# Optimization experiments

Measured on AMD Instinct MI355X. Metric: run time of the kernel, lower is better.

The kernel has to match this reference:

```python
import jax, jax.numpy as jnp
import numpy as np

N_CODES = 1024
CODE_DIM = 64
COMMITMENT_WEIGHT = 0.5
DECAY = 0.99
EPSILON = 1e-05
TEMP = 1.0


def setup_inputs() -> dict:
    key = jax.random.key(0)
    k_z, k_e = jax.random.split(key)
    z = jax.random.normal(k_z, (8, 16384, CODE_DIM), dtype=jnp.float32)
    # xavier_uniform init for embedding [n_codes, code_dim]
    limit = float(np.sqrt(6.0 / (N_CODES + CODE_DIM)))
    embedding = jax.random.uniform(k_e, (N_CODES, CODE_DIM), dtype=jnp.float32,
                                   minval=-limit, maxval=limit)
    ema_cluster_size = jnp.zeros((N_CODES,), dtype=jnp.float32)
    ema_w = embedding.copy()
    return {"z": z, "embedding": embedding,
            "ema_cluster_size": ema_cluster_size, "ema_w": ema_w}


def reference(z, embedding, ema_cluster_size, ema_w):
    lead_shape = z.shape[:-1]
    zf = z.reshape(-1, z.shape[-1])  # [N, D]
    # squared-euclidean distances: ||z||^2 + ||e||^2 - 2 z e^T  -> [N, n_codes]
    d = (jnp.sum(zf * zf, axis=-1, keepdims=True)
         + jnp.sum(embedding * embedding, axis=-1)
         - 2.0 * (zf @ embedding.T)) / TEMP
    idx = jnp.argmin(d, axis=-1)  # [N]
    z_q_f = embedding[idx]        # [N, D]

    # --- EMA codebook update (no-grad buffer math) ---
    ones = jnp.ones_like(idx, dtype=zf.dtype)
    cluster_size = jax.ops.segment_sum(ones, idx, num_segments=N_CODES)      # one_hot.sum(0)
    new_ecs = ema_cluster_size * DECAY + (1.0 - DECAY) * cluster_size
    n = jnp.sum(new_ecs)
    cs = jnp.clip((new_ecs + EPSILON) / (n + N_CODES * EPSILON) * n, 0.01)
    dw = jax.ops.segment_sum(zf, idx, num_segments=N_CODES)                  # one_hot.T @ z
    new_ema_w = ema_w * DECAY + (1.0 - DECAY) * dw
    new_embedding = new_ema_w / cs[:, None]

    # --- losses (straight-through) ---
    z_q = z_q_f.reshape(z.shape)
    commitment_loss = jnp.mean((jax.lax.stop_gradient(z_q) - z) ** 2)
    codebook_loss = jnp.mean((z_q - jax.lax.stop_gradient(z)) ** 2)
    loss = commitment_loss * COMMITMENT_WEIGHT + codebook_loss
    z_q_st = z + jax.lax.stop_gradient(z_q - z)

    # --- perplexity (no-grad) ---
    avg_probs = cluster_size / jnp.sum(cluster_size)
    avg_probs = jnp.clip(avg_probs, 1e-10)
    avg_probs = avg_probs / jnp.sum(avg_probs)
    perplexity = jnp.exp(-jnp.sum(avg_probs * jnp.log(avg_probs)))

    encoding_indices = idx.reshape(lead_shape)
    return (z_q_st, encoding_indices, loss, perplexity,
            new_embedding, new_ecs, new_ema_w)
```

## Files before the change

### kernel.cpp

```cpp
#include <hip/hip_runtime.h>
#include <hip/hip_bf16.h>
#include <math.h>

#define N_ROWS   131072
#define DIMS     64
#define NCODES   1024
#define DECAY    0.99f
#define EPSF     1e-5f
#define BAND     2e-3f

#define OFF_ZQ    0
#define OFF_IDX   8388608
#define OFF_LOSS  8519680
#define OFF_PERP  8519681
#define OFF_EMB   8519682
#define OFF_ECS   8585218
#define OFF_EMAW  8586242

typedef unsigned int uint;
typedef short bf16x8 __attribute__((ext_vector_type(8)));
typedef float f32x4  __attribute__((ext_vector_type(4)));

__device__ __forceinline__ float atomic_add_f32(float* p, float v) {
  return __hip_atomic_fetch_add(p, v, __ATOMIC_RELAXED, __HIP_MEMORY_SCOPE_AGENT);
}

__device__ __forceinline__ unsigned short bf16_rne(float f) {
  uint u = __float_as_uint(f);
  uint r = u + 0x7fffu + ((u >> 16) & 1u);
  return (unsigned short)(r >> 16);
}
__device__ __forceinline__ float bf16_f32(unsigned short h) {
  return __uint_as_float(((uint)h) << 16);
}

__device__ __forceinline__ float np_pairwise64_sq(const float* v) {
#pragma clang fp contract(off)
  float r[8];
#pragma unroll
  for (int j = 0; j < 8; ++j) r[j] = v[j] * v[j];
#pragma unroll
  for (int i = 8; i < 64; i += 8)
#pragma unroll
    for (int j = 0; j < 8; ++j) r[j] += v[i + j] * v[i + j];
  return ((r[0] + r[1]) + (r[2] + r[3])) + ((r[4] + r[5]) + (r[6] + r[7]));
}

__global__ __launch_bounds__(256) void k0m(const float* __restrict__ emb,
                                           float* __restrict__ ee,
                                           uint* __restrict__ cluster,
                                           uint* __restrict__ cnt,
                                           bf16x8* __restrict__ bsplit,
                                           float* __restrict__ dw) {
  int T = blockIdx.x;
  int t = threadIdx.x;
  int gid = T * 256 + t;
  for (int i = gid; i < NCODES * DIMS; i += 16384) dw[i] = 0.0f;

  int l = t & 63;
  int slot = t >> 6;
  int ktile = slot >> 1, split = slot & 1;
  int code = T * 16 + (l & 15);
  int k0 = ktile * 32 + ((l >> 4) << 3);
  const float* ep = emb + (size_t)code * DIMS + k0;
  float4 fa = *(const float4*)ep;
  float4 fb = *(const float4*)(ep + 4);
  float fs[8] = {fa.x, fa.y, fa.z, fa.w, fb.x, fb.y, fb.z, fb.w};
  bf16x8 v;
#pragma unroll
  for (int i = 0; i < 8; ++i) {
    unsigned short h = bf16_rne(fs[i]);
    if (split == 0) v[i] = (short)h;
    else            v[i] = (short)bf16_rne(fs[i] - bf16_f32(h));
  }
  bsplit[(size_t)((T * 2 + ktile) * 2 + split) * 64 + l] = v;

  if (t < 16) {
    int c = T * 16 + t;
    float ev[DIMS];
    const float4* e4 = (const float4*)(emb + (size_t)c * DIMS);
#pragma unroll
    for (int i = 0; i < 16; ++i) {
      float4 w = e4[i];
      ev[4*i] = w.x; ev[4*i+1] = w.y; ev[4*i+2] = w.z; ev[4*i+3] = w.w;
    }
    ee[c] = np_pairwise64_sq(ev);
  } else if (t < 32) {
    cluster[T * 16 + (t - 16)] = 0u;
  }
  if (T == 0 && t == 32) *cnt = 0u;
}

__global__ __launch_bounds__(256) void k1_mfma(const float* __restrict__ z,
                                               const float* __restrict__ emb,
                                               const bf16x8* __restrict__ bsplit,
                                               const float* __restrict__ ee,
                                               int* __restrict__ idx_out,
                                               float* __restrict__ idx_f_out,
                                               float* __restrict__ out_zq,
                                               double* __restrict__ sqpart,
                                               uint* __restrict__ cluster,
                                               uint* __restrict__ cnt,
                                               uint* __restrict__ list) {
  __shared__ float4 btile[4][256];
  __shared__ int    sidx[64];
  __shared__ double wred[4];
  int t = threadIdx.x;
  int l = t & 63;
  int w = t >> 6;
  int rowbase = blockIdx.x * 64 + w * 16;
  int arow = rowbase + (l & 15);
  int kq = (l >> 4) << 3;
  int col = l & 15;

  const float4* bs4 = (const float4*)bsplit;

  bf16x8 ahi[2], ami[2];
#pragma unroll
  for (int t2 = 0; t2 < 2; ++t2) {
    const float* zp = z + (size_t)arow * DIMS + t2 * 32 + kq;
    float4 fa = *(const float4*)zp;
    float4 fb = *(const float4*)(zp + 4);
    float fs[8] = {fa.x, fa.y, fa.z, fa.w, fb.x, fb.y, fb.z, fb.w};
#pragma unroll
    for (int i = 0; i < 8; ++i) {
      unsigned short h = bf16_rne(fs[i]);
      float m = fs[i] - bf16_f32(h);
      ahi[t2][i] = (short)bf16_rne(-2.0f * fs[i]);
      ami[t2][i] = (short)bf16_rne(-2.0f * m);
    }
  }

  float best[4]  = {3.4e38f, 3.4e38f, 3.4e38f, 3.4e38f};
  float second[4] = {3.4e38f, 3.4e38f, 3.4e38f, 3.4e38f};
  int   bidx[4] = {0, 0, 0, 0};

  float4 vp0 = bs4[(size_t)(0 * 4 + w) * 64 + l];
  float4 vp1 = bs4[(size_t)(1 * 4 + w) * 64 + l];
  float4 vp2 = bs4[(size_t)(2 * 4 + w) * 64 + l];
  float4 vp3 = bs4[(size_t)(3 * 4 + w) * 64 + l];

  for (int T = 0; T < 64; T += 4) {
    __syncthreads();
    btile[0][w * 64 + l] = vp0;
    btile[1][w * 64 + l] = vp1;
    btile[2][w * 64 + l] = vp2;
    btile[3][w * 64 + l] = vp3;
    __syncthreads();
    if (T + 4 < 64) {
      vp0 = bs4[(size_t)((T + 4) * 4 + w) * 64 + l];
      vp1 = bs4[(size_t)((T + 5) * 4 + w) * 64 + l];
      vp2 = bs4[(size_t)((T + 6) * 4 + w) * 64 + l];
      vp3 = bs4[(size_t)((T + 7) * 4 + w) * 64 + l];
    }

#pragma unroll
    for (int u = 0; u < 4; ++u) {
      int code = (T + u) * 16 + col;
      float eeT = ee[code];
      bf16x8 bhi0 = __builtin_bit_cast(bf16x8, btile[u][0 * 64 + l]);
      bf16x8 bmi0 = __builtin_bit_cast(bf16x8, btile[u][1 * 64 + l]);
      bf16x8 bhi1 = __builtin_bit_cast(bf16x8, btile[u][2 * 64 + l]);
      bf16x8 bmi1 = __builtin_bit_cast(bf16x8, btile[u][3 * 64 + l]);

      f32x4 acc = {0.f, 0.f, 0.f, 0.f};
      acc = __builtin_amdgcn_mfma_f32_16x16x32_bf16(ahi[0], bhi0, acc, 0, 0, 0);
      acc = __builtin_amdgcn_mfma_f32_16x16x32_bf16(ahi[1], bhi1, acc, 0, 0, 0);
      acc = __builtin_amdgcn_mfma_f32_16x16x32_bf16(ahi[0], bmi0, acc, 0, 0, 0);
      acc = __builtin_amdgcn_mfma_f32_16x16x32_bf16(ahi[1], bmi1, acc, 0, 0, 0);
      acc = __builtin_amdgcn_mfma_f32_16x16x32_bf16(ami[0], bhi0, acc, 0, 0, 0);
      acc = __builtin_amdgcn_mfma_f32_16x16x32_bf16(ami[1], bhi1, acc, 0, 0, 0);

#pragma unroll
      for (int j = 0; j < 4; ++j) {
        float s = acc[j] + eeT;
        bool lt = s < best[j];
        second[j] = lt ? best[j] : fminf(second[j], s);
        best[j]   = lt ? s : best[j];
        bidx[j]   = lt ? code : bidx[j];
      }
    }
  }

#pragma unroll
  for (int m = 1; m < 16; m <<= 1) {
#pragma unroll
    for (int j = 0; j < 4; ++j) {
      float ob = __shfl_xor(best[j], m, 64);
      float os = __shfl_xor(second[j], m, 64);
      int   oi = __shfl_xor(bidx[j], m, 64);
      if (ob < best[j]) {
        second[j] = fminf(os, best[j]);
        best[j] = ob; bidx[j] = oi;
      } else if (ob == best[j]) {
        bidx[j] = min(bidx[j], oi);
        second[j] = fminf(second[j], fminf(os, ob));
      } else {
        second[j] = fminf(second[j], ob);
      }
    }
  }

  if (col == 0) {
#pragma unroll
    for (int j = 0; j < 4; ++j) {
      int lrow = w * 16 + ((l >> 4) << 2) + j;
      int r = blockIdx.x * 64 + lrow;
      sidx[lrow] = bidx[j];
      idx_out[r] = bidx[j];
      idx_f_out[r] = (float)bidx[j];
      atomicAdd(&cluster[bidx[j]], 1u);
      if (second[j] - best[j] < BAND) {
        uint p = atomicAdd(cnt, 1u);
        list[p] = (uint)r;
      }
    }
  }
  __syncthreads();

  double ds = 0.0;
  const float4* z4 = (const float4*)z;
  const float4* e4 = (const float4*)emb;
  float4* zq4 = (float4*)out_zq;
  int blockrow = blockIdx.x * 64;
#pragma unroll
  for (int p = 0; p < 4; ++p) {
    int f = t + p * 256;
    int lrow = f >> 4, d4 = f & 15;
    int code = sidx[lrow];
    float4 zv = z4[(size_t)(blockrow + lrow) * 16 + d4];
    float4 ev = e4[code * 16 + d4];
    float dx = ev.x - zv.x, dy = ev.y - zv.y, dz = ev.z - zv.z, dw_ = ev.w - zv.w;
    float4 o;
    o.x = zv.x + dx; o.y = zv.y + dy; o.z = zv.z + dz; o.w = zv.w + dw_;
    zq4[(size_t)(blockrow + lrow) * 16 + d4] = o;
    float ss = dx * dx + dy * dy + dz * dz + dw_ * dw_;
    ds += (double)ss;
  }
#pragma unroll
  for (int o2 = 32; o2 > 0; o2 >>= 1) ds += __shfl_down(ds, o2, 64);
  if (l == 0) wred[w] = ds;
  __syncthreads();
  if (t == 0) sqpart[blockIdx.x] = (wred[0] + wred[1]) + (wred[2] + wred[3]);
}

__global__ __launch_bounds__(256) void k2_recheck(const float* __restrict__ z,
                                                  const float* __restrict__ emb,
                                                  const float* __restrict__ ee,
                                                  const uint* __restrict__ cnt,
                                                  const uint* __restrict__ list,
                                                  int* __restrict__ idx_out,
                                                  float* __restrict__ idx_f_out,
                                                  float* __restrict__ out_zq,
                                                  uint* __restrict__ cluster,
                                                  double* __restrict__ corr) {
#pragma clang fp contract(off)
  __shared__ float zrow[DIMS];
  __shared__ float rv[256];
  __shared__ int   ri[256];
  __shared__ int   schg, sold, snew;
  int t = threadIdx.x;
  uint n = *cnt;
  double corrAcc = 0.0;
  const float4* e4 = (const float4*)emb;
  float4* zq4 = (float4*)out_zq;

  for (uint i = blockIdx.x; i < n; i += gridDim.x) {
    uint row = list[i];
    __syncthreads();
    if (t < 16)
      ((float4*)zrow)[t] = ((const float4*)(z + (size_t)row * DIMS))[t];
    __syncthreads();
    float zz = np_pairwise64_sq(zrow);
    float best = 3.4e38f; int bi = 0;
#pragma unroll
    for (int k4 = 0; k4 < 4; ++k4) {
      int c = t * 4 + k4;
      const float* e = emb + (size_t)c * DIMS;
      float a = 0.f;
      for (int k = 0; k < DIMS; ++k) a = fmaf(zrow[k], e[k], a);
      float d = fmaf(-2.0f, a, zz + ee[c]);
      if (d < best) { best = d; bi = c; }
    }
    rv[t] = best; ri[t] = bi;
    __syncthreads();
    for (int s = 128; s > 0; s >>= 1) {
      if (t < s) {
        float ov = rv[t + s]; int oi = ri[t + s];
        if (ov < rv[t] || (ov == rv[t] && oi < ri[t])) { rv[t] = ov; ri[t] = oi; }
      }
      __syncthreads();
    }
    if (t == 0) {
      int old = idx_out[row];
      if (ri[0] != old) {
        atomicSub(&cluster[old], 1u);
        atomicAdd(&cluster[ri[0]], 1u);
        idx_out[row] = ri[0];
        idx_f_out[row] = (float)ri[0];
        schg = 1; sold = old; snew = ri[0];
      } else {
        schg = 0;
      }
    }
    __syncthreads();
    if (schg && t < 16) {
      float4 zv = make_float4(zrow[t*4], zrow[t*4+1], zrow[t*4+2], zrow[t*4+3]);
      float4 en = e4[snew * 16 + t];
      float4 eo = e4[sold * 16 + t];
      float dxn = en.x - zv.x, dyn = en.y - zv.y, dzn = en.z - zv.z, dwn = en.w - zv.w;
      float4 o;
      o.x = zv.x + dxn; o.y = zv.y + dyn; o.z = zv.z + dzn; o.w = zv.w + dwn;
      zq4[(size_t)row * 16 + t] = o;
      float ssn = dxn * dxn + dyn * dyn + dzn * dzn + dwn * dwn;
      float dxo = eo.x - zv.x, dyo = eo.y - zv.y, dzo = eo.z - zv.z, dwo = eo.w - zv.w;
      float sso = dxo * dxo + dyo * dyo + dzo * dzo + dwo * dwo;
      double cl = (double)ssn - (double)sso;
      cl += __shfl_xor(cl, 1, 64);
      cl += __shfl_xor(cl, 2, 64);
      cl += __shfl_xor(cl, 4, 64);
      cl += __shfl_xor(cl, 8, 64);
      if (t == 0) corrAcc += cl;
    }
  }
  if (t == 0) corr[blockIdx.x] = corrAcc;
}

__global__ __launch_bounds__(256) void kp(const uint* __restrict__ cluster,
                                          const float* __restrict__ ecs_in,
                                          uint* __restrict__ starts,
                                          uint* __restrict__ cursor,
                                          float* __restrict__ csb,
                                          float* __restrict__ out) {
  __shared__ uint a[256], b[256];
  __shared__ double red[256];
  int t = threadIdx.x;

  uint c0 = cluster[t*4+0], c1 = cluster[t*4+1], c2 = cluster[t*4+2], c3 = cluster[t*4+3];
  uint s4 = c0 + c1 + c2 + c3;
  a[t] = s4;
  __syncthreads();
  uint* src = a; uint* dst = b;
  for (int off = 1; off < 256; off <<= 1) {
    dst[t] = src[t] + ((t >= off) ? src[t - off] : 0u);
    __syncthreads();
    uint* tmp = src; src = dst; dst = tmp;
  }
  uint base = (t > 0) ? src[t-1] : 0u;
  uint p0 = base, p1 = p0 + c0, p2 = p1 + c1, p3 = p2 + c2;
  starts[t*4+0] = p0; starts[t*4+1] = p1; starts[t*4+2] = p2; starts[t*4+3] = p3;
  cursor[t*4+0] = p0; cursor[t*4+1] = p1; cursor[t*4+2] = p2; cursor[t*4+3] = p3;
  if (t == 255) starts[NCODES] = src[255];
  __syncthreads();

  double nloc = 0.0, aloc = 0.0, bloc = 0.0;
  for (int c = t; c < NCODES; c += 256) {
    float cntf = (float)cluster[c];
    float ne = ecs_in[c] * DECAY + (1.0f - DECAY) * cntf;
    out[OFF_ECS + c] = ne;
    nloc += (double)ne;
    double p = (double)cntf / (double)N_ROWS;
    double pc = p < 1e-10 ? 1e-10 : p;
    bloc += pc;
    aloc += pc * log(pc);
  }

  red[t] = nloc; __syncthreads();
  for (int s = 128; s > 0; s >>= 1) { if (t < s) red[t] += red[t + s]; __syncthreads(); }
  double n = red[0]; __syncthreads();

  red[t] = bloc; __syncthreads();
  for (int s = 128; s > 0; s >>= 1) { if (t < s) red[t] += red[t + s]; __syncthreads(); }
  double B = red[0]; __syncthreads();

  red[t] = aloc; __syncthreads();
  for (int s = 128; s > 0; s >>= 1) { if (t < s) red[t] += red[t + s]; __syncthreads(); }
  double A = red[0]; __syncthreads();

  if (t == 0) {
    double ent = -(A / B - log(B));
    out[OFF_PERP] = (float)exp(ent);
  }

  float nf = (float)n;
  for (int c = t; c < NCODES; c += 256) {
    float ne = out[OFF_ECS + c];
    float cs = ((ne + EPSF) / (nf + (float)NCODES * EPSF)) * nf;
    csb[c] = cs < 0.01f ? 0.01f : cs;
  }
}

__global__ __launch_bounds__(256) void k3c_scatter(const int* __restrict__ idx,
                                                   uint* __restrict__ cursor,
                                                   uint* __restrict__ rowids,
                                                   int* __restrict__ codes) {
  int row = blockIdx.x * 256 + threadIdx.x;
  int code = idx[row];
  uint pos = atomicAdd(&cursor[code], 1u);
  rowids[pos] = (uint)row;
  codes[pos] = code;
}

__global__ __launch_bounds__(256) void k3d_dw(const float* __restrict__ z,
                                              const uint* __restrict__ rowids,
                                              const int* __restrict__ codes,
                                              float* __restrict__ dw) {
  int lane = threadIdx.x & 63, w = threadIdx.x >> 6;
  int base = blockIdx.x * 128 + w * 32;

  int cur = codes[base];
  float acc = 0.f;
  for (int i = 0; i < 32; ++i) {
    int p = base + i;
    uint r = rowids[p];
    int c = codes[p];
    if (c != cur) {
      atomic_add_f32(&dw[cur * DIMS + lane], acc);
      acc = 0.f; cur = c;
    }
    acc += z[(size_t)r * DIMS + lane];
  }
  atomic_add_f32(&dw[cur * DIMS + lane], acc);
}

__global__ __launch_bounds__(256) void k4b_emb(const float* __restrict__ emaw_in,
                                               const float* __restrict__ dw,
                                               const float* __restrict__ csb,
                                               const double* __restrict__ sqpart,
                                               const double* __restrict__ corr,
                                               float* __restrict__ out) {
  int i = blockIdx.x * 256 + threadIdx.x;
  int c = i >> 6;
  float nw = emaw_in[i] * DECAY + (1.0f - DECAY) * dw[i];
  out[OFF_EMAW + i] = nw;
  out[OFF_EMB + i] = nw / csb[c];

  if (blockIdx.x == 0) {
    __shared__ double red[256];
    int t = threadIdx.x;
    double sloc = 0.0;
    for (int k = t; k < 2048; k += 256) sloc += sqpart[k];
    for (int k = t; k < 1024; k += 256) sloc += corr[k];
    red[t] = sloc; __syncthreads();
    for (int s = 128; s > 0; s >>= 1) { if (t < s) red[t] += red[t + s]; __syncthreads(); }
    if (t == 0) {
      double M = red[0] / (double)((size_t)N_ROWS * DIMS);
      out[OFF_LOSS] = (float)(1.5 * M);
    }
  }
}

extern "C" void kernel_launch(void* const* d_in, const int* in_sizes, int n_in,
                              void* d_out, int out_size, void* d_ws, size_t ws_size,
                              hipStream_t stream) {
  const float* z    = (const float*)d_in[0];
  const float* emb  = (const float*)d_in[1];
  const float* ecs  = (const float*)d_in[2];
  const float* emaw = (const float*)d_in[3];
  float* out = (float*)d_out;

  char* ws = (char*)d_ws;
  uint*   cnt    = (uint*)   (ws + 0);
  int*    idxw   = (int*)    (ws + 16);
  uint*   clus   = (uint*)   (ws + 524304);
  float*  dw     = (float*)  (ws + 528416);
  float*  ee     = (float*)  (ws + 790560);
  float*  csb    = (float*)  (ws + 794656);
  uint*   starts = (uint*)   (ws + 798752);
  uint*   cursor = (uint*)   (ws + 806944);
  uint*   rowids = (uint*)   (ws + 811040);
  bf16x8* bsplit = (bf16x8*) (ws + 1335328);
  uint*   rlist  = (uint*)   (ws + 1597472);
  int*    codes  = (int*)    (ws + 2121760);
  double* sqpart = (double*) (ws + 2646048);
  double* corr   = (double*) (ws + 2662432);

  k0m<<<64, 256, 0, stream>>>(emb, ee, clus, cnt, bsplit, dw);
  k1_mfma<<<N_ROWS / 64, 256, 0, stream>>>(z, emb, bsplit, ee, idxw,
                                           out + OFF_IDX, out + OFF_ZQ,
                                           sqpart, clus, cnt, rlist);
  k2_recheck<<<1024, 256, 0, stream>>>(z, emb, ee, cnt, rlist, idxw,
                                       out + OFF_IDX, out + OFF_ZQ, clus, corr);
  kp<<<1, 256, 0, stream>>>(clus, ecs, starts, cursor, csb, out);
  k3c_scatter<<<N_ROWS / 256, 256, 0, stream>>>(idxw, cursor, rowids, codes);
  k3d_dw<<<N_ROWS / 128, 256, 0, stream>>>(z, rowids, codes, dw);
  k4b_emb<<<256, 256, 0, stream>>>(emaw, dw, csb, sqpart, corr, out);
}
```

Before: 192.8 us.

## Fuse tail kernels into one cooperative kernel with grid syncs

Replaces the five tail launches (recheck, prefix/stats, scatter, dw accumulation, embedding update) with a single cooperative kernel of 512 blocks that separates phases with grid-wide syncs. This is meant to remove per-launch overhead and the gaps between small dependent kernels. Work is re-partitioned to fit 512 blocks, for example each block handles 256 rows in scatter and 64 rows per wave in dw. If the cooperative launch fails, it falls back to the old launch sequence. The risks are the cost of grid.sync, lower parallelism in some phases, and needing all 512 blocks resident at once.

```diff
diff --git a/kernel.cpp b/kernel.cpp
--- a/kernel.cpp
+++ b/kernel.cpp
@@ -1,6 +1,9 @@
 #include <hip/hip_runtime.h>
 #include <hip/hip_bf16.h>
+#include <hip/hip_cooperative_groups.h>
 #include <math.h>
+
+namespace cg = cooperative_groups;
 
 #define N_ROWS   131072
 #define DIMS     64
@@ -244,6 +247,205 @@
   if (t == 0) sqpart[blockIdx.x] = (wred[0] + wred[1]) + (wred[2] + wred[3]);
 }
 
+struct TailArgs {
+  const float* z; const float* emb; const float* ee;
+  const float* ecs_in; const float* emaw_in;
+  uint* cnt; uint* list; int* idxw; float* idx_f; float* out_zq;
+  uint* cluster; double* corr; uint* starts; uint* cursor; float* csb;
+  uint* rowids; int* codes; float* dw; double* sqpart; float* out;
+};
+
+__global__ __launch_bounds__(256, 2) void ktail(TailArgs A) {
+#pragma clang fp contract(off)
+  cg::grid_group grid = cg::this_grid();
+  int t = threadIdx.x;
+  int b = blockIdx.x;
+
+  {
+    __shared__ float zrow[DIMS];
+    __shared__ float rv[256];
+    __shared__ int   ri[256];
+    __shared__ int   schg, sold, snew;
+    uint n = *A.cnt;
+    double corrAcc = 0.0;
+    const float4* e4 = (const float4*)A.emb;
+    float4* zq4 = (float4*)A.out_zq;
+
+    for (uint i = (uint)b; i < n; i += gridDim.x) {
+      uint row = A.list[i];
+      __syncthreads();
+      if (t < 16)
+        ((float4*)zrow)[t] = ((const float4*)(A.z + (size_t)row * DIMS))[t];
+      __syncthreads();
+      float zz = np_pairwise64_sq(zrow);
+      float best = 3.4e38f; int bi = 0;
+#pragma unroll
+      for (int k4 = 0; k4 < 4; ++k4) {
+        int c = t * 4 + k4;
+        const float* e = A.emb + (size_t)c * DIMS;
+        float a = 0.f;
+        for (int k = 0; k < DIMS; ++k) a = fmaf(zrow[k], e[k], a);
+        float d = fmaf(-2.0f, a, zz + A.ee[c]);
+        if (d < best) { best = d; bi = c; }
+      }
+      rv[t] = best; ri[t] = bi;
+      __syncthreads();
+      for (int s = 128; s > 0; s >>= 1) {
+        if (t < s) {
+          float ov = rv[t + s]; int oi = ri[t + s];
+          if (ov < rv[t] || (ov == rv[t] && oi < ri[t])) { rv[t] = ov; ri[t] = oi; }
+        }
+        __syncthreads();
+      }
+      if (t == 0) {
+        int old = A.idxw[row];
+        if (ri[0] != old) {
+          atomicSub(&A.cluster[old], 1u);
+          atomicAdd(&A.cluster[ri[0]], 1u);
+          A.idxw[row] = ri[0];
+          A.idx_f[row] = (float)ri[0];
+          schg = 1; sold = old; snew = ri[0];
+        } else {
+          schg = 0;
+        }
+      }
+      __syncthreads();
+      if (schg && t < 16) {
+        float4 zv = make_float4(zrow[t*4], zrow[t*4+1], zrow[t*4+2], zrow[t*4+3]);
+        float4 en = e4[snew * 16 + t];
+        float4 eo = e4[sold * 16 + t];
+        float dxn = en.x - zv.x, dyn = en.y - zv.y, dzn = en.z - zv.z, dwn = en.w - zv.w;
+        float4 o;
+        o.x = zv.x + dxn; o.y = zv.y + dyn; o.z = zv.z + dzn; o.w = zv.w + dwn;
+        zq4[(size_t)row * 16 + t] = o;
+        float ssn = dxn * dxn + dyn * dyn + dzn * dzn + dwn * dwn;
+        float dxo = eo.x - zv.x, dyo = eo.y - zv.y, dzo = eo.z - zv.z, dwo = eo.w - zv.w;
+        float sso = dxo * dxo + dyo * dyo + dzo * dzo + dwo * dwo;
+        double cl = (double)ssn - (double)sso;
+        cl += __shfl_xor(cl, 1, 64);
+        cl += __shfl_xor(cl, 2, 64);
+        cl += __shfl_xor(cl, 4, 64);
+        cl += __shfl_xor(cl, 8, 64);
+        if (t == 0) corrAcc += cl;
+      }
+    }
+    if (t == 0) A.corr[b] = corrAcc;
+  }
+  grid.sync();
+
+  if (b == 0) {
+    __shared__ uint a[256], bb[256];
+    __shared__ double red[256];
+
+    uint c0 = A.cluster[t*4+0], c1 = A.cluster[t*4+1],
+         c2 = A.cluster[t*4+2], c3 = A.cluster[t*4+3];
+    uint s4 = c0 + c1 + c2 + c3;
+    a[t] = s4;
+    __syncthreads();
+    uint* src = a; uint* dst = bb;
+    for (int off = 1; off < 256; off <<= 1) {
+      dst[t] = src[t] + ((t >= off) ? src[t - off] : 0u);
+      __syncthreads();
+      uint* tmp = src; src = dst; dst = tmp;
+    }
+    uint base = (t > 0) ? src[t-1] : 0u;
+    uint p0 = base, p1 = p0 + c0, p2 = p1 + c1, p3 = p2 + c2;
+    A.starts[t*4+0] = p0; A.starts[t*4+1] = p1;
+    A.starts[t*4+2] = p2; A.starts[t*4+3] = p3;
+    A.cursor[t*4+0] = p0; A.cursor[t*4+1] = p1;
+    A.cursor[t*4+2] = p2; A.cursor[t*4+3] = p3;
+    if (t == 255) A.starts[NCODES] = src[255];
+    __syncthreads();
+
+    double nloc = 0.0, aloc = 0.0, bloc = 0.0;
+    for (int c = t; c < NCODES; c += 256) {
+      float cntf = (float)A.cluster[c];
+      float ne = A.ecs_in[c] * DECAY + (1.0f - DECAY) * cntf;
+      A.out[OFF_ECS + c] = ne;
+      nloc += (double)ne;
+      double p = (double)cntf / (double)N_ROWS;
+      double pc = p < 1e-10 ? 1e-10 : p;
+      bloc += pc;
+      aloc += pc * log(pc);
+    }
+
+    red[t] = nloc; __syncthreads();
+    for (int s = 128; s > 0; s >>= 1) { if (t < s) red[t] += red[t + s]; __syncthreads(); }
+    double n = red[0]; __syncthreads();
+
+    red[t] = bloc; __syncthreads();
+    for (int s = 128; s > 0; s >>= 1) { if (t < s) red[t] += red[t + s]; __syncthreads(); }
+    double B = red[0]; __syncthreads();
+
+    red[t] = aloc; __syncthreads();
+    for (int s = 128; s > 0; s >>= 1) { if (t < s) red[t] += red[t + s]; __syncthreads(); }
+    double Aa = red[0]; __syncthreads();
+
+    if (t == 0) {
+      double ent = -(Aa / B - log(B));
+      A.out[OFF_PERP] = (float)exp(ent);
+    }
+
+    float nf = (float)n;
+    for (int c = t; c < NCODES; c += 256) {
+      float ne = A.out[OFF_ECS + c];
+      float cs = ((ne + EPSF) / (nf + (float)NCODES * EPSF)) * nf;
+      A.csb[c] = cs < 0.01f ? 0.01f : cs;
+    }
+  }
+  grid.sync();
+
+  {
+    int row = b * 256 + t;
+    int code = A.idxw[row];
+    uint pos = atomicAdd(&A.cursor[code], 1u);
+    A.rowids[pos] = (uint)row;
+    A.codes[pos] = code;
+  }
+  grid.sync();
+
+  {
+    int lane = t & 63, w = t >> 6;
+    int base = b * 256 + w * 64;
+    int cur = A.codes[base];
+    float acc = 0.f;
+    for (int i = 0; i < 64; ++i) {
+      int p = base + i;
+      uint r = A.rowids[p];
+      int c = A.codes[p];
+      if (c != cur) {
+        atomic_add_f32(&A.dw[cur * DIMS + lane], acc);
+        acc = 0.f; cur = c;
+      }
+      acc += A.z[(size_t)r * DIMS + lane];
+    }
+    atomic_add_f32(&A.dw[cur * DIMS + lane], acc);
+  }
+  grid.sync();
+
+  {
+    if (t < 128) {
+      int i = b * 128 + t;
+      int c = i >> 6;
+      float nw = A.emaw_in[i] * DECAY + (1.0f - DECAY) * A.dw[i];
+      A.out[OFF_EMAW + i] = nw;
+      A.out[OFF_EMB + i] = nw / A.csb[c];
+    }
+    if (b == 0) {
+      __shared__ double red[256];
+      double sloc = 0.0;
+      for (int k = t; k < 2048; k += 256) sloc += A.sqpart[k];
+      for (int k = t; k < 512; k += 256) sloc += A.corr[k];
+      red[t] = sloc; __syncthreads();
+      for (int s = 128; s > 0; s >>= 1) { if (t < s) red[t] += red[t + s]; __syncthreads(); }
+      if (t == 0) {
+        double M = red[0] / (double)((size_t)N_ROWS * DIMS);
+        A.out[OFF_LOSS] = (float)(1.5 * M);
+      }
+    }
+  }
+}
+
 __global__ __launch_bounds__(256) void k2_recheck(const float* __restrict__ z,
                                                   const float* __restrict__ emb,
                                                   const float* __restrict__ ee,
@@ -479,10 +681,25 @@
   k1_mfma<<<N_ROWS / 64, 256, 0, stream>>>(z, emb, bsplit, ee, idxw,
                                            out + OFF_IDX, out + OFF_ZQ,
                                            sqpart, clus, cnt, rlist);
-  k2_recheck<<<1024, 256, 0, stream>>>(z, emb, ee, cnt, rlist, idxw,
-                                       out + OFF_IDX, out + OFF_ZQ, clus, corr);
-  kp<<<1, 256, 0, stream>>>(clus, ecs, starts, cursor, csb, out);
-  k3c_scatter<<<N_ROWS / 256, 256, 0, stream>>>(idxw, cursor, rowids, codes);
-  k3d_dw<<<N_ROWS / 128, 256, 0, stream>>>(z, rowids, codes, dw);
-  k4b_emb<<<256, 256, 0, stream>>>(emaw, dw, csb, sqpart, corr, out);
-}
+
+  TailArgs ta;
+  ta.z = z; ta.emb = emb; ta.ee = ee; ta.ecs_in = ecs; ta.emaw_in = emaw;
+  ta.cnt = cnt; ta.list = rlist; ta.idxw = idxw; ta.idx_f = out + OFF_IDX;
+  ta.out_zq = out + OFF_ZQ; ta.cluster = clus; ta.corr = corr;
+  ta.starts = starts; ta.cursor = cursor; ta.csb = csb;
+  ta.rowids = rowids; ta.codes = codes; ta.dw = dw; ta.sqpart = sqpart;
+  ta.out = out;
+  void* kargs[] = { &ta };
+  hipError_t cerr = hipLaunchCooperativeKernel((void*)ktail, dim3(512),
+                                               dim3(256), kargs, 0, stream);
+  if (cerr != hipSuccess) {
+    (void)hipGetLastError();
+    k2_recheck<<<1024, 256, 0, stream>>>(z, emb, ee, cnt, rlist, idxw,
+                                         out + OFF_IDX, out + OFF_ZQ, clus,
+                                         corr);
+    kp<<<1, 256, 0, stream>>>(clus, ecs, starts, cursor, csb, out);
+    k3c_scatter<<<N_ROWS / 256, 256, 0, stream>>>(idxw, cursor, rowids, codes);
+    k3d_dw<<<N_ROWS / 128, 256, 0, stream>>>(z, rowids, codes, dw);
+    k4b_emb<<<256, 256, 0, stream>>>(emaw, dw, csb, sqpart, corr, out);
+  }
+}
```

Result: slower. 451.7 us (+134.3%).
